# Kernel tuning notes

Hardware: AMD Instinct MI355X
Metric: run time of the kernel (lower is better)

Reference implementation:

```python
import jax, jax.numpy as jnp
import numpy as np

B, S, D, H = 2, 2048, 4096, 32
HD = D // H
FF = 22016 // 2  # QWenMLP gets intermediate_size // 2 = 11008
EPS = 1e-6
THETA = 10000.0


def setup_inputs() -> dict:
    key = jax.random.key(0)
    ks = jax.random.split(key, 10)
    s = lambda fan_in: 1.0 / np.sqrt(fan_in)
    return {
        "positions": jnp.broadcast_to(jnp.arange(S, dtype=jnp.int32), (B, S)),
        "hidden_states": jax.random.normal(ks[0], (B, S, D), jnp.float32),
        "ln1_w": jnp.ones((D,), jnp.float32),
        "ln2_w": jnp.ones((D,), jnp.float32),
        "Wqkv": jax.random.normal(ks[1], (D, 3 * D), jnp.float32) * s(D),
        "bqkv": jax.random.normal(ks[2], (3 * D,), jnp.float32) * 0.02,
        "Wo": jax.random.normal(ks[3], (D, D), jnp.float32) * s(D),
        "W1": jax.random.normal(ks[4], (D, FF), jnp.float32) * s(D),
        "W2": jax.random.normal(ks[5], (D, FF), jnp.float32) * s(D),
        "Wout": jax.random.normal(ks[6], (FF, D), jnp.float32) * s(FF),
    }


def _rmsnorm(x, w, eps=EPS):
    return x * jax.lax.rsqrt(jnp.mean(x * x, axis=-1, keepdims=True) + eps) * w


def _rope(x, positions):
    # x: [B, S, H, HD]; NeoX-style rotate-half RoPE over full head_dim
    inv_freq = 1.0 / (THETA ** (jnp.arange(0, HD, 2, dtype=jnp.float32) / HD))
    freqs = positions.astype(jnp.float32)[..., None] * inv_freq  # [B, S, HD/2]
    cos = jnp.concatenate([jnp.cos(freqs)] * 2, axis=-1)[:, :, None, :]
    sin = jnp.concatenate([jnp.sin(freqs)] * 2, axis=-1)[:, :, None, :]
    x1, x2 = jnp.split(x, 2, axis=-1)
    rotated = jnp.concatenate([-x2, x1], axis=-1)
    return x * cos + rotated * sin


def reference(positions, hidden_states, ln1_w, ln2_w, Wqkv, bqkv, Wo, W1, W2, Wout):
    residual = hidden_states
    h = _rmsnorm(hidden_states, ln1_w)
    qkv = h @ Wqkv + bqkv                              # [B, S, 3D]
    q, k, v = jnp.split(qkv, 3, axis=-1)
    q = _rope(q.reshape(B, S, H, HD), positions)
    k = _rope(k.reshape(B, S, H, HD), positions)
    v = v.reshape(B, S, H, HD)
    scores = jnp.einsum("bqhd,bkhd->bhqk", q, k) * (HD ** -0.5)
    causal = jnp.tril(jnp.ones((S, S), bool))
    scores = jnp.where(causal, scores, jnp.finfo(scores.dtype).min)
    probs = jax.nn.softmax(scores, axis=-1)
    attn = jnp.einsum("bhqk,bkhd->bqhd", probs, v).reshape(B, S, D)
    h = residual + attn @ Wo
    residual = h
    h = _rmsnorm(h, ln2_w)
    h = (h @ W1) * jax.nn.silu(h @ W2)                  # SwiGLU: w1(x) * silu(w2(x))
    return residual + h @ Wout
```

## Files before the change

kernel.cpp:

```cpp
#include <hip/hip_runtime.h>

typedef unsigned short u16;
typedef unsigned int   u32;
typedef __bf16 bf16x8 __attribute__((ext_vector_type(8)));
typedef float  f32x4  __attribute__((ext_vector_type(4)));
typedef unsigned short u16x4 __attribute__((ext_vector_type(4)));
typedef unsigned short u16x8 __attribute__((ext_vector_type(8)));

#define DEV __device__ __forceinline__

DEV u16 f2b(float f) {
  u32 u = __builtin_bit_cast(u32, f);
  return (u16)((u + 0x7fffu + ((u >> 16) & 1u)) >> 16);
}
DEV float b2f(u16 h) { u32 u = ((u32)h) << 16; return __builtin_bit_cast(float, u); }

DEV void gload16(const void* g, void* l) {
  __builtin_amdgcn_global_load_lds((__attribute__((address_space(1))) void*)(g),
                                   (__attribute__((address_space(3))) void*)(l),
                                   16, 0, 0);
}

DEV f32x4 MFMA(bf16x8 a, bf16x8 b, f32x4 c) {
  return __builtin_amdgcn_mfma_f32_16x16x32_bf16(a, b, c, 0, 0, 0);
}

__global__ __launch_bounds__(256) void transpose_cvt(const float* __restrict__ W,
                                                     u16* __restrict__ Wt,
                                                     int K, int N) {
  __shared__ float tile[32][33];
  const int n0 = blockIdx.x * 32, k0 = blockIdx.y * 32;
  const int tx = threadIdx.x, ty = threadIdx.y;
#pragma unroll
  for (int i = 0; i < 32; i += 8)
    tile[ty + i][tx] = W[(size_t)(k0 + ty + i) * N + n0 + tx];
  __syncthreads();
#pragma unroll
  for (int i = 0; i < 32; i += 8)
    Wt[(size_t)(n0 + ty + i) * K + k0 + tx] = f2b(tile[tx][ty + i]);
}

__global__ __launch_bounds__(256) void rmsnorm_k(const float* __restrict__ x,
                                                 const float* __restrict__ w,
                                                 u16* __restrict__ o, int D) {
  const int row = blockIdx.x, tid = threadIdx.x;
  const float4* xr = (const float4*)(x + (size_t)row * D);
  const float4* wr = (const float4*)w;
  float4 v[4];
  float ss = 0.f;
#pragma unroll
  for (int i = 0; i < 4; ++i) {
    v[i] = xr[i * 256 + tid];
    ss += v[i].x * v[i].x + v[i].y * v[i].y + v[i].z * v[i].z + v[i].w * v[i].w;
  }
#pragma unroll
  for (int off = 1; off < 64; off <<= 1) ss += __shfl_xor(ss, off, 64);
  __shared__ float red[4];
  if ((tid & 63) == 0) red[tid >> 6] = ss;
  __syncthreads();
  const float tot = red[0] + red[1] + red[2] + red[3];
  const float sc = rsqrtf(tot / (float)D + 1e-6f);
  u16x4* orow = (u16x4*)(o + (size_t)row * D);
#pragma unroll
  for (int i = 0; i < 4; ++i) {
    float4 wv = wr[i * 256 + tid];
    u16x4 p;
    p[0] = f2b(v[i].x * sc * wv.x);
    p[1] = f2b(v[i].y * sc * wv.y);
    p[2] = f2b(v[i].z * sc * wv.z);
    p[3] = f2b(v[i].w * sc * wv.w);
    orow[i * 256 + tid] = p;
  }
}

__global__ __launch_bounds__(256) void rope_table(const int* __restrict__ positions,
                                                  float* __restrict__ tab, int BS) {
  const int idx = blockIdx.x * 256 + threadIdx.x;
  if (idx >= BS * 64) return;
  const int bs = idx >> 6, i = idx & 63;
  const float pos = (float)positions[bs];
  const float inv = __expf(-(float)i * (9.210340371976184f / 64.f));
  const float ang = pos * inv;
  float s, c;
  sincosf(ang, &s, &c);
  tab[idx] = c;
  tab[BS * 64 + idx] = s;
}

__global__ __launch_bounds__(256) void rope_apply(u16* __restrict__ qkv,
                                                  const float* __restrict__ tab, int BS) {
  const int idx = blockIdx.x * 256 + threadIdx.x;
  if (idx >= BS * 2048) return;
  const int i = idx & 63, h = (idx >> 6) & 31, bs = idx >> 11;
  const float c = tab[bs * 64 + i];
  const float s = tab[(size_t)BS * 64 + bs * 64 + i];
  const size_t base = (size_t)bs * 12288 + h * 128 + i;
  float x1 = b2f(qkv[base]), x2 = b2f(qkv[base + 64]);
  qkv[base] = f2b(x1 * c - x2 * s);
  qkv[base + 64] = f2b(x2 * c + x1 * s);
  float y1 = b2f(qkv[base + 4096]), y2 = b2f(qkv[base + 4096 + 64]);
  qkv[base + 4096] = f2b(y1 * c - y2 * s);
  qkv[base + 4096 + 64] = f2b(y2 * c + y1 * s);
}

template <int MODE>
__global__ __launch_bounds__(512, 2) void gemm256(const u16* __restrict__ A,
                                                  const u16* __restrict__ Bt,
                                                  void* __restrict__ outp,
                                                  const float* __restrict__ bias,
                                                  const float* __restrict__ resid,
                                                  const u16* __restrict__ g1,
                                                  int M, int N, int K) {
  __shared__ __align__(16) u16 A0s[256 * 32], A1s[256 * 32];
  __shared__ __align__(16) u16 B0s[256 * 32], B1s[256 * 32];
  const int tid = threadIdx.x;
  const int wid = tid >> 6, l = tid & 63;
  const int wm = wid >> 2, wn = wid & 3;
  const int lr = l & 15, lc = l >> 4;
  const int gx = gridDim.x;
  const int nwg = gx * gridDim.y;
  const int orig = blockIdx.y * gx + blockIdx.x;
  const int wg = (orig & 7) * (nwg >> 3) + (orig >> 3);
  const int m0 = (wg / gx) * 256, n0 = (wg % gx) * 256;

  const int NT = K >> 6;
  const int rt = tid >> 2;
  const int ct = (tid & 3) ^ (rt & 3);
  const u16* aS = A + (size_t)(m0 + rt) * K + ct * 8;
  const u16* bS = Bt + (size_t)(n0 + rt) * K + ct * 8;

  auto STG = [&](u16* reg, const u16* src, int koff) {
    gload16(src + koff, reg + wid * 512);
    gload16(src + (size_t)128 * K + koff, reg + 4096 + wid * 512);
  };
  auto RA = [&](const u16* reg, int mf) {
    const int r = wm * 128 + mf * 16 + lr;
    return *(const bf16x8*)&reg[r * 32 + ((lc ^ (r & 3)) * 8)];
  };
  auto RB = [&](const u16* reg, int nf) {
    const int r = wn * 64 + nf * 16 + lr;
    return *(const bf16x8*)&reg[r * 32 + ((lc ^ (r & 3)) * 8)];
  };

  f32x4 acc[8][4] = {};

#define BAR() asm volatile("s_barrier" ::: "memory")
#define VM2() asm volatile("s_waitcnt vmcnt(2)" ::: "memory")

  STG(A0s, aS, 0);
  STG(B0s, bS, 0);
  STG(A1s, aS, 32);
  VM2();
  BAR();

  for (int t = 0; t < NT; ++t) {
    const int k0 = t << 6, k1 = (t + 1) << 6;
    bf16x8 afr[8], bq0, bq1;
#pragma unroll
    for (int mf = 0; mf < 8; ++mf) afr[mf] = RA(A0s, mf);
    bq0 = RB(B0s, 0); bq1 = RB(B0s, 1);
    STG(B1s, bS, k0 + 32);
    BAR();
    __builtin_amdgcn_s_setprio(1);
#pragma unroll
    for (int mf = 0; mf < 8; ++mf) {
      acc[mf][0] = MFMA(afr[mf], bq0, acc[mf][0]);
      acc[mf][1] = MFMA(afr[mf], bq1, acc[mf][1]);
    }
    __builtin_amdgcn_s_setprio(0);
    BAR();
    bq0 = RB(B0s, 2); bq1 = RB(B0s, 3);
    if (t + 1 < NT) STG(A0s, aS, k1);
    BAR();
    __builtin_amdgcn_s_setprio(1);
#pragma unroll
    for (int mf = 0; mf < 8; ++mf) {
      acc[mf][2] = MFMA(afr[mf], bq0, acc[mf][2]);
      acc[mf][3] = MFMA(afr[mf], bq1, acc[mf][3]);
    }
    __builtin_amdgcn_s_setprio(0);
    VM2();
    BAR();
#pragma unroll
    for (int mf = 0; mf < 8; ++mf) afr[mf] = RA(A1s, mf);
    bq0 = RB(B1s, 0); bq1 = RB(B1s, 1);
    if (t + 1 < NT) STG(B0s, bS, k1);
    BAR();
    __builtin_amdgcn_s_setprio(1);
#pragma unroll
    for (int mf = 0; mf < 8; ++mf) {
      acc[mf][0] = MFMA(afr[mf], bq0, acc[mf][0]);
      acc[mf][1] = MFMA(afr[mf], bq1, acc[mf][1]);
    }
    __builtin_amdgcn_s_setprio(0);
    BAR();
    bq0 = RB(B1s, 2); bq1 = RB(B1s, 3);
    if (t + 1 < NT) STG(A1s, aS, k1 + 32);
    BAR();
    __builtin_amdgcn_s_setprio(1);
#pragma unroll
    for (int mf = 0; mf < 8; ++mf) {
      acc[mf][2] = MFMA(afr[mf], bq0, acc[mf][2]);
      acc[mf][3] = MFMA(afr[mf], bq1, acc[mf][3]);
    }
    __builtin_amdgcn_s_setprio(0);
    VM2();
    BAR();
  }
#undef BAR
#undef VM2

#pragma unroll
  for (int mf = 0; mf < 8; ++mf) {
#pragma unroll
    for (int nf = 0; nf < 4; ++nf) {
      const int gr = m0 + wm * 128 + mf * 16 + lc * 4;
      const int gc = n0 + wn * 64 + nf * 16 + lr;
#pragma unroll
      for (int r = 0; r < 4; ++r) {
        float v = acc[mf][nf][r];
        const size_t idx = (size_t)(gr + r) * N + gc;
        if constexpr (MODE == 0) {
          ((u16*)outp)[idx] = f2b(v);
        } else if constexpr (MODE == 1) {
          ((u16*)outp)[idx] = f2b(v + bias[gc]);
        } else if constexpr (MODE == 2) {
          ((float*)outp)[idx] = v + resid[idx];
        } else {
          const float g = b2f(g1[idx]);
          const float sv = v / (1.f + __expf(-v));
          ((u16*)outp)[idx] = f2b(g * sv);
        }
      }
    }
  }
}

__global__ __launch_bounds__(256) void attn_kernel(const u16* __restrict__ qkv,
                                                   u16* __restrict__ o, int S) {
  const int qtile = gridDim.x - 1 - blockIdx.x;
  const int bh = blockIdx.y;
  const int b = bh >> 5, h = bh & 31;
  const int q0 = qtile * 64;
  const int tid = threadIdx.x;
  const int w = tid >> 6, l = tid & 63;
  const int lr = l & 15, lc = l >> 4;
  const size_t RS = 12288;
  const float SCALE = 0.08838834764831845f;

  __shared__ __align__(16) u16 Ks[64 * 128];
  __shared__ __align__(16) u16 Vt[128 * 64];
  __shared__ __align__(16) u16 Ps[4][16 * 64];

  bf16x8 qf[4];
  {
    const u16* qp = qkv + (size_t)(b * S + q0 + w * 16 + lr) * RS + h * 128 + 8 * lc;
#pragma unroll
    for (int kc = 0; kc < 4; ++kc) qf[kc] = *(const bf16x8*)(qp + kc * 32);
  }

  float m_[4], ls[4];
  f32x4 O[8] = {};
#pragma unroll
  for (int r = 0; r < 4; ++r) { m_[r] = -3e38f; ls[r] = 0.f; }

  const int nkt = qtile + 1;
  for (int kt = 0; kt < nkt; ++kt) {
    const int k0 = kt * 64;
#pragma unroll
    for (int it = 0; it < 4; ++it) {
      const int eid = it * 256 + tid;
      const int kr = eid >> 4, d0 = (eid & 15) * 8;
      u16x8 k8 = *(const u16x8*)(qkv + (size_t)(b * S + k0 + kr) * RS + 4096 + h * 128 + d0);
      *(u16x8*)&Ks[kr * 128 + (d0 ^ ((kr & 7) * 8))] = k8;
    }
#pragma unroll
    for (int it = 0; it < 4; ++it) {
      const int d0 = (it * 4 + w) * 8;
      u16x8 v8 = *(const u16x8*)(qkv + (size_t)(b * S + k0 + l) * RS + 8192 + h * 128 + d0);
#pragma unroll
      for (int jj = 0; jj < 8; ++jj) {
        const int d = d0 + jj;
        Vt[(d * 64 + l) ^ ((d & 7) * 8)] = v8[jj];
      }
    }
    __syncthreads();

    const int nks = (kt == qtile) ? (w + 1) : 4;
    float sv[4][4];
#pragma unroll
    for (int ks = 0; ks < 4; ++ks) {
      if (ks < nks) {
        const int row = ks * 16 + lr;
        f32x4 sacc = {0.f, 0.f, 0.f, 0.f};
#pragma unroll
        for (int kc = 0; kc < 4; ++kc) {
          bf16x8 kf = *(const bf16x8*)&Ks[row * 128 + ((kc * 32 + 8 * lc) ^ ((lr & 7) * 8))];
          sacc = MFMA(qf[kc], kf, sacc);
        }
        const bool dm = (kt == qtile) && (ks == w);
#pragma unroll
        for (int r = 0; r < 4; ++r) {
          float x = sacc[r] * SCALE;
          if (dm) {
            const int kg = ks * 16 + lr, qg = w * 16 + lc * 4 + r;
            if (kg > qg) x = -3e38f;
          }
          sv[ks][r] = x;
        }
      } else {
#pragma unroll
        for (int r = 0; r < 4; ++r) sv[ks][r] = -3e38f;
      }
    }

    float alpha[4];
#pragma unroll
    for (int r = 0; r < 4; ++r) {
      float pm = fmaxf(fmaxf(sv[0][r], sv[1][r]), fmaxf(sv[2][r], sv[3][r]));
#pragma unroll
      for (int off = 1; off < 16; off <<= 1) pm = fmaxf(pm, __shfl_xor(pm, off, 64));
      const float mn = fmaxf(m_[r], pm);
      alpha[r] = __expf(m_[r] - mn);
      m_[r] = mn;
    }
    float p[4][4];
#pragma unroll
    for (int ks = 0; ks < 4; ++ks)
#pragma unroll
      for (int r = 0; r < 4; ++r) {
        p[ks][r] = __expf(sv[ks][r] - m_[r]);
        const int q = lc * 4 + r, k = ks * 16 + lr;
        Ps[w][q * 64 + (k ^ ((q & 7) * 8))] = f2b(p[ks][r]);
      }
#pragma unroll
    for (int r = 0; r < 4; ++r) {
      float s = p[0][r] + p[1][r] + p[2][r] + p[3][r];
#pragma unroll
      for (int off = 1; off < 16; off <<= 1) s += __shfl_xor(s, off, 64);
      ls[r] = ls[r] * alpha[r] + s;
    }
#pragma unroll
    for (int dt = 0; dt < 8; ++dt)
#pragma unroll
      for (int r = 0; r < 4; ++r) O[dt][r] *= alpha[r];

#pragma unroll
    for (int half = 0; half < 2; ++half) {
      const bf16x8 ap = *(const bf16x8*)&Ps[w][lr * 64 + ((half * 32 + 8 * lc) ^ ((lr & 7) * 8))];
#pragma unroll
      for (int dt = 0; dt < 8; ++dt) {
        const int d = dt * 16 + lr;
        const bf16x8 bv = *(const bf16x8*)&Vt[d * 64 + ((half * 32 + 8 * lc) ^ ((d & 7) * 8))];
        O[dt] = MFMA(ap, bv, O[dt]);
      }
    }
    __syncthreads();
  }

  float inv[4];
#pragma unroll
  for (int r = 0; r < 4; ++r) inv[r] = 1.f / ls[r];
#pragma unroll
  for (int dt = 0; dt < 8; ++dt)
#pragma unroll
    for (int r = 0; r < 4; ++r) {
      const int qg = q0 + w * 16 + lc * 4 + r;
      o[(size_t)(b * S + qg) * 4096 + h * 128 + dt * 16 + lr] = f2b(O[dt][r] * inv[r]);
    }
}

extern "C" void kernel_launch(void* const* d_in, const int* in_sizes, int n_in,
                              void* d_out, int out_size, void* d_ws, size_t ws_size,
                              hipStream_t stream) {
  const int*   positions = (const int*)d_in[0];
  const float* hidden    = (const float*)d_in[1];
  const float* ln1       = (const float*)d_in[2];
  const float* ln2       = (const float*)d_in[3];
  const float* Wqkv      = (const float*)d_in[4];
  const float* bqkv      = (const float*)d_in[5];
  const float* Wo        = (const float*)d_in[6];
  const float* W1        = (const float*)d_in[7];
  const float* W2        = (const float*)d_in[8];
  const float* Wout      = (const float*)d_in[9];
  float* out = (float*)d_out;

  const int S = 2048, BS = 4096, D = 4096, FF = 11008, N3 = 12288;

  char* ws = (char*)d_ws;
  size_t off = 0;
  auto alloc = [&](size_t bytes) { void* p = ws + off; off += (bytes + 255) & ~(size_t)255; return p; };
  u16*   WT    = (u16*)alloc((size_t)N3 * D * 2);
  u16*   qkv   = (u16*)alloc((size_t)BS * N3 * 2);
  u16*   slotH = (u16*)alloc((size_t)BS * D * 2);
  float* h2    = (float*)alloc((size_t)BS * D * 4);
  u16*   slotG = (u16*)alloc((size_t)BS * FF * 2);
  float* tab   = (float*)alloc((size_t)2 * BS * 64 * 4);
  if (ws_size < off) return;

  rope_table<<<(BS * 64 + 255) / 256, 256, 0, stream>>>(positions, tab, BS);

  transpose_cvt<<<dim3(N3 / 32, D / 32), dim3(32, 8), 0, stream>>>(Wqkv, WT, D, N3);
  rmsnorm_k<<<BS, 256, 0, stream>>>(hidden, ln1, slotH, D);
  gemm256<1><<<dim3(N3 / 256, BS / 256), 512, 0, stream>>>(slotH, WT, qkv, bqkv, nullptr, nullptr, BS, N3, D);
  rope_apply<<<(BS * 2048) / 256, 256, 0, stream>>>(qkv, tab, BS);

  attn_kernel<<<dim3(S / 64, 64), 256, 0, stream>>>(qkv, slotH, S);

  transpose_cvt<<<dim3(D / 32, D / 32), dim3(32, 8), 0, stream>>>(Wo, WT, D, D);
  gemm256<2><<<dim3(D / 256, BS / 256), 512, 0, stream>>>(slotH, WT, h2, nullptr, hidden, nullptr, BS, D, D);

  rmsnorm_k<<<BS, 256, 0, stream>>>(h2, ln2, slotH, D);
  transpose_cvt<<<dim3(FF / 32, D / 32), dim3(32, 8), 0, stream>>>(W1, WT, D, FF);
  gemm256<0><<<dim3(FF / 256, BS / 256), 512, 0, stream>>>(slotH, WT, slotG, nullptr, nullptr, nullptr, BS, FF, D);
  transpose_cvt<<<dim3(FF / 32, D / 32), dim3(32, 8), 0, stream>>>(W2, WT, D, FF);
  gemm256<3><<<dim3(FF / 256, BS / 256), 512, 0, stream>>>(slotH, WT, slotG, nullptr, nullptr, slotG, BS, FF, D);
  transpose_cvt<<<dim3(D / 32, FF / 32), dim3(32, 8), 0, stream>>>(Wout, WT, FF, D);
  gemm256<2><<<dim3(D / 256, BS / 256), 512, 0, stream>>>(slotG, WT, out, nullptr, h2, nullptr, BS, D, FF);
}
```

Measured before the change: 2.474 ms.

## Triple-buffer GEMM LDS tiles with a rotating slot pipeline

Replaces the two fixed A/B LDS double buffers with three rotating 32-wide K slots. Tiles are now prefetched two steps ahead, so the wait only needs to allow four outstanding loads. The LDS swizzle also changes from row&3 to (row>>1)&3 to alter the bank-conflict pattern. The risk is LDS footprint: it rises from 64KB to 96KB per block, which may no longer let the two blocks per CU requested by the launch bounds fit.

```diff
diff --git a/kernel.cpp b/kernel.cpp
--- a/kernel.cpp
+++ b/kernel.cpp
@@ -111,8 +111,8 @@
                                                   const float* __restrict__ resid,
                                                   const u16* __restrict__ g1,
                                                   int M, int N, int K) {
-  __shared__ __align__(16) u16 A0s[256 * 32], A1s[256 * 32];
-  __shared__ __align__(16) u16 B0s[256 * 32], B1s[256 * 32];
+  __shared__ __align__(16) u16 As[3 * 8192];
+  __shared__ __align__(16) u16 Bs[3 * 8192];
   const int tid = threadIdx.x;
   const int wid = tid >> 6, l = tid & 63;
   const int wm = wid >> 2, wn = wid & 3;
@@ -123,92 +123,100 @@
   const int wg = (orig & 7) * (nwg >> 3) + (orig >> 3);
   const int m0 = (wg / gx) * 256, n0 = (wg % gx) * 256;
 
-  const int NT = K >> 6;
+  const int NT = K >> 5;
+  const int NI = NT >> 1;
+
   const int rt = tid >> 2;
-  const int ct = (tid & 3) ^ (rt & 3);
+  const int ct = (tid & 3) ^ ((rt >> 1) & 3);
   const u16* aS = A + (size_t)(m0 + rt) * K + ct * 8;
   const u16* bS = Bt + (size_t)(n0 + rt) * K + ct * 8;
 
-  auto STG = [&](u16* reg, const u16* src, int koff) {
-    gload16(src + koff, reg + wid * 512);
-    gload16(src + (size_t)128 * K + koff, reg + 4096 + wid * 512);
+  auto STG = [&](u16* slot, const u16* src, int tk) {
+    gload16(src + tk * 32, slot + wid * 512);
+    gload16(src + (size_t)128 * K + tk * 32, slot + 4096 + wid * 512);
   };
-  auto RA = [&](const u16* reg, int mf) {
+  auto RA = [&](const u16* slot, int mf) {
     const int r = wm * 128 + mf * 16 + lr;
-    return *(const bf16x8*)&reg[r * 32 + ((lc ^ (r & 3)) * 8)];
+    return *(const bf16x8*)&slot[r * 32 + ((lc ^ ((r >> 1) & 3)) * 8)];
   };
-  auto RB = [&](const u16* reg, int nf) {
+  auto RB = [&](const u16* slot, int nf) {
     const int r = wn * 64 + nf * 16 + lr;
-    return *(const bf16x8*)&reg[r * 32 + ((lc ^ (r & 3)) * 8)];
+    return *(const bf16x8*)&slot[r * 32 + ((lc ^ ((r >> 1) & 3)) * 8)];
   };
 
   f32x4 acc[8][4] = {};
 
 #define BAR() asm volatile("s_barrier" ::: "memory")
-#define VM2() asm volatile("s_waitcnt vmcnt(2)" ::: "memory")
-
-  STG(A0s, aS, 0);
-  STG(B0s, bS, 0);
-  STG(A1s, aS, 32);
-  VM2();
+#define VM4() asm volatile("s_waitcnt vmcnt(4)" ::: "memory")
+
+  STG(&As[0], aS, 0);
+  STG(&Bs[0], bS, 0);
+  STG(&As[8192], aS, 1);
+  STG(&Bs[8192], bS, 1);
+  VM4();
   BAR();
 
-  for (int t = 0; t < NT; ++t) {
-    const int k0 = t << 6, k1 = (t + 1) << 6;
-    bf16x8 afr[8], bq0, bq1;
-#pragma unroll
-    for (int mf = 0; mf < 8; ++mf) afr[mf] = RA(A0s, mf);
-    bq0 = RB(B0s, 0); bq1 = RB(B0s, 1);
-    STG(B1s, bS, k0 + 32);
+  int sa = 0, sb = 1, sc = 2;
+  for (int i = 0; i < NI; ++i) {
+    const int Tc = 2 * i + 2, Td = 2 * i + 3;
+    u16* Aa = &As[sa * 8192]; u16* Ba = &Bs[sa * 8192];
+    u16* Ab = &As[sb * 8192]; u16* Bb = &Bs[sb * 8192];
+    u16* Ac = &As[sc * 8192]; u16* Bc = &Bs[sc * 8192];
+    bf16x8 af[8], b0, b1;
+#pragma unroll
+    for (int mf = 0; mf < 8; ++mf) af[mf] = RA(Aa, mf);
+    b0 = RB(Ba, 0); b1 = RB(Ba, 1);
+    if (Tc < NT) STG(Ac, aS, Tc);
     BAR();
     __builtin_amdgcn_s_setprio(1);
 #pragma unroll
     for (int mf = 0; mf < 8; ++mf) {
-      acc[mf][0] = MFMA(afr[mf], bq0, acc[mf][0]);
-      acc[mf][1] = MFMA(afr[mf], bq1, acc[mf][1]);
+      acc[mf][0] = MFMA(af[mf], b0, acc[mf][0]);
+      acc[mf][1] = MFMA(af[mf], b1, acc[mf][1]);
     }
     __builtin_amdgcn_s_setprio(0);
     BAR();
-    bq0 = RB(B0s, 2); bq1 = RB(B0s, 3);
-    if (t + 1 < NT) STG(A0s, aS, k1);
+    b0 = RB(Ba, 2); b1 = RB(Ba, 3);
+    if (Tc < NT) STG(Bc, bS, Tc);
     BAR();
     __builtin_amdgcn_s_setprio(1);
 #pragma unroll
     for (int mf = 0; mf < 8; ++mf) {
-      acc[mf][2] = MFMA(afr[mf], bq0, acc[mf][2]);
-      acc[mf][3] = MFMA(afr[mf], bq1, acc[mf][3]);
+      acc[mf][2] = MFMA(af[mf], b0, acc[mf][2]);
+      acc[mf][3] = MFMA(af[mf], b1, acc[mf][3]);
     }
     __builtin_amdgcn_s_setprio(0);
-    VM2();
-    BAR();
-#pragma unroll
-    for (int mf = 0; mf < 8; ++mf) afr[mf] = RA(A1s, mf);
-    bq0 = RB(B1s, 0); bq1 = RB(B1s, 1);
-    if (t + 1 < NT) STG(B0s, bS, k1);
+    VM4();
+    BAR();
+#pragma unroll
+    for (int mf = 0; mf < 8; ++mf) af[mf] = RA(Ab, mf);
+    b0 = RB(Bb, 0); b1 = RB(Bb, 1);
+    if (Td < NT) STG(Aa, aS, Td);
     BAR();
     __builtin_amdgcn_s_setprio(1);
 #pragma unroll
     for (int mf = 0; mf < 8; ++mf) {
-      acc[mf][0] = MFMA(afr[mf], bq0, acc[mf][0]);
-      acc[mf][1] = MFMA(afr[mf], bq1, acc[mf][1]);
+      acc[mf][0] = MFMA(af[mf], b0, acc[mf][0]);
+      acc[mf][1] = MFMA(af[mf], b1, acc[mf][1]);
     }
     __builtin_amdgcn_s_setprio(0);
     BAR();
-    bq0 = RB(B1s, 2); bq1 = RB(B1s, 3);
-    if (t + 1 < NT) STG(A1s, aS, k1 + 32);
+    b0 = RB(Bb, 2); b1 = RB(Bb, 3);
+    if (Td < NT) STG(Ba, bS, Td);
     BAR();
     __builtin_amdgcn_s_setprio(1);
 #pragma unroll
     for (int mf = 0; mf < 8; ++mf) {
-      acc[mf][2] = MFMA(afr[mf], bq0, acc[mf][2]);
-      acc[mf][3] = MFMA(afr[mf], bq1, acc[mf][3]);
+      acc[mf][2] = MFMA(af[mf], b0, acc[mf][2]);
+      acc[mf][3] = MFMA(af[mf], b1, acc[mf][3]);
     }
     __builtin_amdgcn_s_setprio(0);
-    VM2();
-    BAR();
+    VM4();
+    BAR();
+    const int t = sc; sc = sb; sb = sa; sa = t;
   }
 #undef BAR
-#undef VM2
+#undef VM4
 
 #pragma unroll
   for (int mf = 0; mf < 8; ++mf) {
```

Measured after the change: 2.387 ms. 3.5% less time.
